# Kernel tuning notes

Hardware: AMD Instinct MI355X
Metric: run time of the kernel (lower is better)

Reference implementation:

```python
import jax, jax.numpy as jnp
import numpy as np

BETA = 0.05
KNN = 6
UL_ALPHA = 0.05
UL_BETA = 1.0


def setup_inputs() -> dict:
    key = jax.random.key(0)
    k1, k2, k3 = jax.random.split(key, 3)
    B, D, N = 256, 2048, 16384
    inputs = jax.random.normal(k1, (B, D), dtype=jnp.float32)
    em = jax.random.normal(k2, (N, D), dtype=jnp.float32)
    # exemplar memory rows are kept unit-norm by the update rule
    em = em / jnp.linalg.norm(em, axis=1, keepdims=True)
    targets = jax.random.randint(k3, (B,), 0, N, dtype=jnp.int64)
    return {"inputs": inputs, "em": em, "targets": targets, "epoch": 10}


def smooth_hot(logits, targets, em, k):
    # Vectorized k-reciprocal neighbor search (replaces the per-sample Python loop).
    m, n = logits.shape
    # index_sorted[:, :k] == top-k class indices per sample
    _, topk_idx = jax.lax.top_k(logits, k)            # [m, k]
    neigh = em[topk_idx]                               # [m, k, d]
    sims = jnp.einsum('mkd,nd->mkn', neigh, em)        # [m, k, n]
    _, neigh_topk = jax.lax.top_k(sims, k)             # [m, k, k]
    # neighbor j of sample i is reciprocal if anchor (top-1 of i) is in its top-k
    anchor = topk_idx[:, :1, None]                     # [m, 1, 1]
    recip = (neigh_topk == anchor).any(axis=-1)        # [m, k]
    weights = jnp.where(recip, 3.0 / k, 0.0).astype(logits.dtype)
    rows = jnp.arange(m)[:, None]
    onehot = jnp.zeros_like(logits).at[rows, topk_idx].set(weights)
    onehot = onehot.at[jnp.arange(m), targets].set(1.0)
    return onehot


def reference(inputs, em, targets, epoch):
    # ExemplarMemory.forward: similarity logits against the memory bank
    logits = (inputs @ em.T) / BETA                    # [B, N]
    # epoch >= 5 and knn > 0 branch (epoch=10)
    onehot = jax.lax.stop_gradient(
        smooth_hot(jax.lax.stop_gradient(logits), targets, em, KNN))
    logp = jax.nn.log_softmax(logits, axis=1)
    beta_loss = (-(onehot * logp).sum(axis=1)).mean()
    t_re = jnp.where(onehot == 0.0, jnp.float32(1e-4), onehot)
    alpha_loss = (-(jax.nn.softmax(logits, axis=1) * jnp.log(t_re)).sum(axis=1)).mean()
    return (UL_ALPHA * alpha_loss, UL_BETA * beta_loss)
```

## Files before the change

kernel.cpp:

```cpp
#include <hip/hip_runtime.h>
#include <math.h>

#define DIMK 2048
#define NEMB 16384
#define NB 256
#define NR2 1536
#define INV_BETA 20.0f
#define NEG_INF (-3.0e38f)

typedef short short8 __attribute__((ext_vector_type(8)));
typedef float f32x4 __attribute__((ext_vector_type(4)));

__device__ __forceinline__ unsigned short f2bf(float f) {
  unsigned u = __float_as_uint(f);
  u += 0x7fffu + ((u >> 16) & 1u);
  return (unsigned short)(u >> 16);
}

__device__ __forceinline__ void ins6i(float x, int xi, float v[6], int vi[6]) {
  if (x > v[5] || (x == v[5] && xi < vi[5])) {
    v[5] = x; vi[5] = xi;
#pragma unroll
    for (int j = 5; j > 0; j--) {
      if (v[j] > v[j - 1] || (v[j] == v[j - 1] && vi[j] < vi[j - 1])) {
        float tv = v[j]; v[j] = v[j - 1]; v[j - 1] = tv;
        int ti = vi[j]; vi[j] = vi[j - 1]; vi[j - 1] = ti;
      }
    }
  }
}

__global__ __launch_bounds__(256) void cvt_kernel(const float* __restrict__ src,
                                                  unsigned short* __restrict__ dst, int n4) {
  int i = blockIdx.x * 256 + threadIdx.x;
  if (i < n4) {
    float4 f = ((const float4*)src)[i];
    ushort4 o;
    o.x = f2bf(f.x); o.y = f2bf(f.y); o.z = f2bf(f.z); o.w = f2bf(f.w);
    ((ushort4*)dst)[i] = o;
  }
}

template <int MODE>
__global__ __launch_bounds__(256, 3) void gemm_rs(
    const unsigned short* __restrict__ Abase, const unsigned short* __restrict__ Bbase,
    const int* __restrict__ nidx, float* __restrict__ outC,
    const float* __restrict__ saIn, int* __restrict__ cntOut,
    const int* __restrict__ surv, const int* __restrict__ nsurvp) {
  constexpr int MTILE = (MODE == 0) ? 64 : 128;
  constexpr int MI = 4;
  constexpr int NI = (MODE == 0) ? 2 : 4;
  constexpr int NSUB_A = MTILE / 16;
  constexpr int NSUB = NSUB_A + 8;
  constexpr int NA = NSUB / 4;
  constexpr int NK = DIMK / 32;

  __shared__ unsigned short st[2][NSUB * 512];
  __shared__ int rowIdxSh[128];
  __shared__ float saSh[128];
  __shared__ int cntSh[128];
  __shared__ int outRowSh[128];
  int t = threadIdx.x;
  int lane = t & 63, wave = t >> 6;
  int quad = lane >> 4, l16 = lane & 15;
  int wr = (MODE == 0) ? 0 : (wave >> 1);
  int wc = (MODE == 0) ? wave : (wave & 1);
  int bn = blockIdx.x, bm = blockIdx.y;
  int nvalid = 128;

  if constexpr (MODE == 2) {
    int ns = nsurvp[0];
    if (bm * 128 >= ns) return;
    nvalid = (ns - bm * 128 < 128) ? (ns - bm * 128) : 128;
  }
  if constexpr (MODE >= 1) {
    if (t < 128) {
      int r;
      if constexpr (MODE == 1) r = bm * 128 + t;
      else r = surv[bm * 128 + ((t < nvalid) ? t : 0)];
      rowIdxSh[t] = nidx[r];
      saSh[t] = saIn[r];
      cntSh[t] = 0;
      outRowSh[t] = r;
    }
    __syncthreads();
  }

  int colbase = (MODE == 2) ? ((bn + 16) * 128) : (bn * 128);

  const unsigned short* agp[NA];
  int soff[NA];
  {
    int seg = lane >> 4;
#pragma unroll
    for (int a = 0; a < NA; a++) {
      int s = wave + a * 4;
      size_t grow;
      const unsigned short* basep;
      if (s < NSUB_A) {
        int r = s * 16 + l16;
        grow = (MODE == 0) ? (size_t)(bm * MTILE + r) : (size_t)rowIdxSh[r];
        basep = Abase;
      } else {
        grow = (size_t)(colbase + (s - NSUB_A) * 16 + l16);
        basep = Bbase;
      }
      agp[a] = basep + grow * DIMK + seg * 8;
      soff[a] = s * 512;
    }
  }

  f32x4 acc[MI][NI];
#pragma unroll
  for (int mi = 0; mi < MI; mi++)
#pragma unroll
    for (int ni = 0; ni < NI; ni++) acc[mi][ni] = (f32x4)0.0f;

  int lo = lane * 8;

  short8 rA[NA], rB2[NA];
  auto LOADT = [&](short8* R, int kk) {
#pragma unroll
    for (int a = 0; a < NA; a++) R[a] = *(const short8*)(agp[a] + kk * 32);
  };
  auto WRITET = [&](const short8* R, int b) {
#pragma unroll
    for (int a = 0; a < NA; a++) *(short8*)&st[b][soff[a] + lo] = R[a];
  };
  auto COMPUTE = [&](int b) {
    const unsigned short* hb = &st[b][0];
    short8 af[MI], bfv[NI];
#pragma unroll
    for (int mi = 0; mi < MI; mi++)
      af[mi] = *(const short8*)&hb[(wr * MI + mi) * 512 + lo];
#pragma unroll
    for (int ni = 0; ni < NI; ni++)
      bfv[ni] = *(const short8*)&hb[(NSUB_A + wc * NI + ni) * 512 + lo];
#pragma unroll
    for (int mi = 0; mi < MI; mi++)
#pragma unroll
      for (int ni = 0; ni < NI; ni++)
        acc[mi][ni] =
            __builtin_amdgcn_mfma_f32_16x16x32_bf16(af[mi], bfv[ni], acc[mi][ni], 0, 0, 0);
  };

  LOADT(rA, 0);
  LOADT(rB2, 1);
  WRITET(rA, 0);
  __syncthreads();

  for (int k = 0; k < NK; k += 2) {
    if (k + 2 < NK) LOADT(rA, k + 2);
    COMPUTE(0);
    WRITET(rB2, 1);
    __syncthreads();
    if (k + 3 < NK) LOADT(rB2, k + 3);
    COMPUTE(1);
    if (k + 2 < NK) WRITET(rA, 0);
    __syncthreads();
  }

  if constexpr (MODE == 0) {
#pragma unroll
    for (int mi = 0; mi < MI; mi++) {
      int row = bm * MTILE + mi * 16 + quad * 4;
#pragma unroll
      for (int ni = 0; ni < NI; ni++) {
        int col = bn * 128 + wave * 32 + ni * 16 + l16;
#pragma unroll
        for (int rr = 0; rr < 4; rr++)
          outC[(size_t)(row + rr) * NEMB + col] = acc[mi][ni][rr] * INV_BETA;
      }
    }
  } else {
#pragma unroll
    for (int mi = 0; mi < MI; mi++) {
#pragma unroll
      for (int rr = 0; rr < 4; rr++) {
        int rloc = wr * 64 + mi * 16 + quad * 4 + rr;
        float s = saSh[rloc];
        int c = 0;
#pragma unroll
        for (int ni = 0; ni < NI; ni++) c += (acc[mi][ni][rr] > s) ? 1 : 0;
        c += __shfl_xor(c, 1, 64);
        c += __shfl_xor(c, 2, 64);
        c += __shfl_xor(c, 4, 64);
        c += __shfl_xor(c, 8, 64);
        if (l16 == 0) atomicAdd(&cntSh[rloc], c);
      }
    }
    __syncthreads();
    if (t < nvalid) atomicAdd(&cntOut[outRowSh[t]], cntSh[t]);
  }
}

__global__ __launch_bounds__(256) void compact_kernel(const int* __restrict__ cnt,
                                                      int* __restrict__ surv,
                                                      int* __restrict__ nsurv) {
  __shared__ int ctr;
  if (threadIdx.x == 0) ctr = 0;
  __syncthreads();
  for (int i = threadIdx.x; i < NR2; i += 256) {
    if (cnt[i] < 6) {
      int p = atomicAdd(&ctr, 1);
      surv[p] = i;
    }
  }
  __syncthreads();
  if (threadIdx.x == 0) nsurv[0] = ctr;
}

__global__ __launch_bounds__(1024) void rowstats_kernel(
    const float* __restrict__ logits, float* __restrict__ topv,
    int* __restrict__ topi, float* __restrict__ lse) {
  int m = blockIdx.x, t = threadIdx.x;
  const float4* row4 = (const float4*)(logits + (size_t)m * NEMB);
  float v6[6]; int i6[6];
#pragma unroll
  for (int j = 0; j < 6; j++) { v6[j] = NEG_INF; i6[j] = 0x7fffffff; }
  float vals[16];
#pragma unroll
  for (int j = 0; j < 4; j++) {
    float4 f = row4[t + j * 1024];
    vals[j * 4 + 0] = f.x; vals[j * 4 + 1] = f.y;
    vals[j * 4 + 2] = f.z; vals[j * 4 + 3] = f.w;
  }
  float mx = vals[0];
#pragma unroll
  for (int r = 1; r < 16; r++) mx = fmaxf(mx, vals[r]);
  float sme = 0.f;
#pragma unroll
  for (int r = 0; r < 16; r++) sme += expf(vals[r] - mx);
#pragma unroll
  for (int j = 0; j < 4; j++) {
    int base = (t + j * 1024) * 4;
#pragma unroll
    for (int b = 0; b < 4; b++) ins6i(vals[j * 4 + b], base + b, v6, i6);
  }
  __shared__ float sv[1024 * 6]; __shared__ int si[1024 * 6];
  __shared__ float smx[1024], ssm[1024];
#pragma unroll
  for (int j = 0; j < 6; j++) { sv[t * 6 + j] = v6[j]; si[t * 6 + j] = i6[j]; }
  smx[t] = mx; ssm[t] = sme;
  __syncthreads();
  for (int s = 512; s > 0; s >>= 1) {
    if (t < s) {
      float mo = smx[t + s], lo2 = ssm[t + s];
      float mn = fmaxf(smx[t], mo);
      ssm[t] = ssm[t] * expf(smx[t] - mn) + lo2 * expf(mo - mn);
      smx[t] = mn;
#pragma unroll
      for (int j = 0; j < 6; j++) ins6i(sv[(t + s) * 6 + j], si[(t + s) * 6 + j], v6, i6);
#pragma unroll
      for (int j = 0; j < 6; j++) { sv[t * 6 + j] = v6[j]; si[t * 6 + j] = i6[j]; }
    }
    __syncthreads();
  }
  if (t == 0) {
    lse[m] = smx[0] + logf(ssm[0]);
#pragma unroll
    for (int j = 0; j < 6; j++) { topv[m * 6 + j] = v6[j]; topi[m * 6 + j] = i6[j]; }
  }
}

__global__ __launch_bounds__(256) void sa_kernel(const float* __restrict__ em,
                                                 const int* __restrict__ topi,
                                                 float* __restrict__ sa,
                                                 int* __restrict__ cnt) {
  int gid = blockIdx.x * 256 + threadIdx.x;
  int w = gid >> 6, lane = gid & 63;
  if (w >= NR2) return;
  if (lane == 1) cnt[w] = 0;
  int m = w / 6;
  int i = topi[w], a = topi[m * 6];
  const float* ei = em + (size_t)i * DIMK;
  const float* ea = em + (size_t)a * DIMK;
  float s = 0.f;
  for (int d = lane; d < DIMK; d += 64) s += ei[d] * ea[d];
#pragma unroll
  for (int off = 32; off > 0; off >>= 1) s += __shfl_down(s, off, 64);
  if (lane == 0) sa[w] = s;
}

__global__ __launch_bounds__(256) void final_kernel(
    const float* __restrict__ logits, const float* __restrict__ topv,
    const int* __restrict__ topi, const float* __restrict__ lse_arr,
    const int* __restrict__ cnt, const int* __restrict__ targets,
    float* __restrict__ out) {
  int m = threadIdx.x;
  float lse = lse_arr[m];
  int tgt = targets[m];
  float tl = logits[(size_t)m * NEMB + tgt];
  float beta = 0.f, Ps = 0.f, nbp = 0.f;
  bool tin = false;
#pragma unroll
  for (int k = 0; k < 6; k++) {
    int idx = topi[m * 6 + k]; float v = topv[m * 6 + k];
    float p = expf(v - lse);
    if (idx == tgt) { tin = true; beta += (lse - v); Ps += p; }
    else if (cnt[m * 6 + k] < 6) { beta += 0.5f * (lse - v); Ps += p; nbp += p; }
  }
  if (!tin) { beta += (lse - tl); Ps += expf(tl - lse); }
  float alpha = 9.2103404f * (1.f - Ps) + 0.6931472f * nbp;
  __shared__ float sA[256], sB2[256];
  sA[m] = alpha; sB2[m] = beta;
  __syncthreads();
  for (int s = 128; s > 0; s >>= 1) {
    if (m < s) { sA[m] += sA[m + s]; sB2[m] += sB2[m + s]; }
    __syncthreads();
  }
  if (m == 0) { out[0] = 0.05f * sA[0] / 256.f; out[1] = sB2[0] / 256.f; }
}

extern "C" void kernel_launch(void* const* d_in, const int* in_sizes, int n_in,
                              void* d_out, int out_size, void* d_ws, size_t ws_size,
                              hipStream_t stream) {
  const float* x = (const float*)d_in[0];
  const float* em = (const float*)d_in[1];
  const int* targets = (const int*)d_in[2];
  char* ws = (char*)d_ws;
  unsigned short* em_bf = (unsigned short*)ws;
  unsigned short* x_bf  = (unsigned short*)(ws + 67108864);
  float* logits = (float*)(ws + 68157440);
  int*   cnt    = (int*)  (ws + 84934656);
  int*   surv   = (int*)  (ws + 84940800);
  int*   nsurv  = (int*)  (ws + 84946944);
  float* topv   = (float*)(ws + 89653248);
  int*   topi   = (int*)  (ws + 89659392);
  float* lse    = (float*)(ws + 89665536);
  float* sa     = (float*)(ws + 89666560);

  cvt_kernel<<<dim3(32768), dim3(256), 0, stream>>>(em, em_bf, NEMB * DIMK / 4);
  cvt_kernel<<<dim3(512), dim3(256), 0, stream>>>(x, x_bf, NB * DIMK / 4);
  gemm_rs<0><<<dim3(128, 4), dim3(256), 0, stream>>>(
      x_bf, em_bf, (const int*)nullptr, logits, (const float*)nullptr, (int*)nullptr,
      (const int*)nullptr, (const int*)nullptr);
  rowstats_kernel<<<dim3(256), dim3(1024), 0, stream>>>(logits, topv, topi, lse);
  sa_kernel<<<dim3(384), dim3(256), 0, stream>>>(em, topi, sa, cnt);
  gemm_rs<1><<<dim3(16, 12), dim3(256), 0, stream>>>(
      em_bf, em_bf, topi, (float*)nullptr, sa, cnt, (const int*)nullptr,
      (const int*)nullptr);
  compact_kernel<<<dim3(1), dim3(256), 0, stream>>>(cnt, surv, nsurv);
  gemm_rs<2><<<dim3(112, 12), dim3(256), 0, stream>>>(
      em_bf, em_bf, topi, (float*)nullptr, sa, cnt, surv, nsurv);
  final_kernel<<<dim3(1), dim3(256), 0, stream>>>(logits, topv, topi, lse, cnt, targets,
                                                  (float*)d_out);
}
```

Baseline: 409.9 us.

## Split-K the three GEMMs with partial-sum planes and separate reduce/count kernels

Each GEMM now splits the K dimension across blockIdx.z (2, 4, and 2 slices) and writes fp32 partial results to separate planes instead of reducing in registers. New countA/countB kernels sum the partials and do the threshold counting, and rowstats sums the two logit planes and also captures the target logit. The goal is more blocks in flight for the small-grid GEMMs (192 blocks in mode 1) so the GPU is better filled. The cost is large extra global-memory traffic for the partial planes (hundreds of MB of workspace) plus extra kernel launches.

Result: slower. 468.1 us (+14.2%).

```diff
diff --git a/kernel.cpp b/kernel.cpp
--- a/kernel.cpp
+++ b/kernel.cpp
@@ -42,10 +42,9 @@
 }
 
 template <int MODE>
-__global__ __launch_bounds__(256, 3) void gemm_rs(
+__global__ __launch_bounds__(256, 3) void gemm_ks(
     const unsigned short* __restrict__ Abase, const unsigned short* __restrict__ Bbase,
-    const int* __restrict__ nidx, float* __restrict__ outC,
-    const float* __restrict__ saIn, int* __restrict__ cntOut,
+    const int* __restrict__ nidx, float* __restrict__ outP,
     const int* __restrict__ surv, const int* __restrict__ nsurvp) {
   constexpr int MTILE = (MODE == 0) ? 64 : 128;
   constexpr int MI = 4;
@@ -53,40 +52,36 @@
   constexpr int NSUB_A = MTILE / 16;
   constexpr int NSUB = NSUB_A + 8;
   constexpr int NA = NSUB / 4;
-  constexpr int NK = DIMK / 32;
+  constexpr int NKC = (MODE == 1) ? 16 : 32;
+  constexpr int OSTRIDE = (MODE == 0) ? 16384 : ((MODE == 1) ? 2048 : 14336);
+  constexpr size_t PLANE = (size_t)((MODE == 0) ? 256 : 1536) * OSTRIDE;
 
   __shared__ unsigned short st[2][NSUB * 512];
   __shared__ int rowIdxSh[128];
-  __shared__ float saSh[128];
-  __shared__ int cntSh[128];
-  __shared__ int outRowSh[128];
   int t = threadIdx.x;
   int lane = t & 63, wave = t >> 6;
   int quad = lane >> 4, l16 = lane & 15;
   int wr = (MODE == 0) ? 0 : (wave >> 1);
   int wc = (MODE == 0) ? wave : (wave & 1);
-  int bn = blockIdx.x, bm = blockIdx.y;
-  int nvalid = 128;
+  int bn = blockIdx.x, bm = blockIdx.y, kz = blockIdx.z;
 
   if constexpr (MODE == 2) {
     int ns = nsurvp[0];
     if (bm * 128 >= ns) return;
-    nvalid = (ns - bm * 128 < 128) ? (ns - bm * 128) : 128;
-  }
-  if constexpr (MODE >= 1) {
     if (t < 128) {
-      int r;
-      if constexpr (MODE == 1) r = bm * 128 + t;
-      else r = surv[bm * 128 + ((t < nvalid) ? t : 0)];
+      int idx = bm * 128 + t;
+      int r = surv[(idx < ns) ? idx : (bm * 128)];
       rowIdxSh[t] = nidx[r];
-      saSh[t] = saIn[r];
-      cntSh[t] = 0;
-      outRowSh[t] = r;
-    }
+    }
+    __syncthreads();
+  }
+  if constexpr (MODE == 1) {
+    if (t < 128) rowIdxSh[t] = nidx[bm * 128 + t];
     __syncthreads();
   }
 
   int colbase = (MODE == 2) ? ((bn + 16) * 128) : (bn * 128);
+  int kbase = kz * (NKC * 32);
 
   const unsigned short* agp[NA];
   int soff[NA];
@@ -105,7 +100,7 @@
         grow = (size_t)(colbase + (s - NSUB_A) * 16 + l16);
         basep = Bbase;
       }
-      agp[a] = basep + grow * DIMK + seg * 8;
+      agp[a] = basep + grow * DIMK + kbase + seg * 8;
       soff[a] = s * 512;
     }
   }
@@ -148,18 +143,18 @@
   LOADT(rB2, 1);
   WRITET(rA, 0);
   __syncthreads();
-
-  for (int k = 0; k < NK; k += 2) {
-    if (k + 2 < NK) LOADT(rA, k + 2);
+  for (int k = 0; k < NKC; k += 2) {
+    if (k + 2 < NKC) LOADT(rA, k + 2);
     COMPUTE(0);
     WRITET(rB2, 1);
     __syncthreads();
-    if (k + 3 < NK) LOADT(rB2, k + 3);
+    if (k + 3 < NKC) LOADT(rB2, k + 3);
     COMPUTE(1);
-    if (k + 2 < NK) WRITET(rA, 0);
-    __syncthreads();
-  }
-
+    if (k + 2 < NKC) WRITET(rA, 0);
+    __syncthreads();
+  }
+
+  float* op = outP + (size_t)kz * PLANE;
   if constexpr (MODE == 0) {
 #pragma unroll
     for (int mi = 0; mi < MI; mi++) {
@@ -169,28 +164,59 @@
         int col = bn * 128 + wave * 32 + ni * 16 + l16;
 #pragma unroll
         for (int rr = 0; rr < 4; rr++)
-          outC[(size_t)(row + rr) * NEMB + col] = acc[mi][ni][rr] * INV_BETA;
+          op[(size_t)(row + rr) * OSTRIDE + col] = acc[mi][ni][rr] * INV_BETA;
       }
     }
   } else {
 #pragma unroll
     for (int mi = 0; mi < MI; mi++) {
 #pragma unroll
-      for (int rr = 0; rr < 4; rr++) {
-        int rloc = wr * 64 + mi * 16 + quad * 4 + rr;
-        float s = saSh[rloc];
-        int c = 0;
-#pragma unroll
-        for (int ni = 0; ni < NI; ni++) c += (acc[mi][ni][rr] > s) ? 1 : 0;
-        c += __shfl_xor(c, 1, 64);
-        c += __shfl_xor(c, 2, 64);
-        c += __shfl_xor(c, 4, 64);
-        c += __shfl_xor(c, 8, 64);
-        if (l16 == 0) atomicAdd(&cntSh[rloc], c);
+      for (int ni = 0; ni < NI; ni++) {
+        int col = bn * 128 + wc * 64 + ni * 16 + l16;
+#pragma unroll
+        for (int rr = 0; rr < 4; rr++) {
+          int row = bm * 128 + wr * 64 + mi * 16 + quad * 4 + rr;
+          op[(size_t)row * OSTRIDE + col] = acc[mi][ni][rr];
+        }
       }
     }
-    __syncthreads();
-    if (t < nvalid) atomicAdd(&cntOut[outRowSh[t]], cntSh[t]);
+  }
+}
+
+__global__ __launch_bounds__(256) void countA_kernel(const float* __restrict__ simsA,
+                                                     const float* __restrict__ sa,
+                                                     int* __restrict__ cnt) {
+  int t = threadIdx.x, lane = t & 63;
+  constexpr size_t PL = (size_t)1536 * 2048;
+  for (int it = blockIdx.x; it < 1536 * 8; it += 256) {
+    int row = it >> 3, cx = it & 7;
+    size_t o = (size_t)row * 2048 + cx * 256 + t;
+    float s = simsA[o] + simsA[o + PL] + simsA[o + 2 * PL] + simsA[o + 3 * PL];
+    int c = (s > sa[row]) ? 1 : 0;
+#pragma unroll
+    for (int off = 32; off > 0; off >>= 1) c += __shfl_down(c, off, 64);
+    if (lane == 0 && c > 0) atomicAdd(&cnt[row], c);
+  }
+}
+
+__global__ __launch_bounds__(256) void countB_kernel(const float* __restrict__ simsB,
+                                                     const float* __restrict__ sa,
+                                                     const int* __restrict__ surv,
+                                                     const int* __restrict__ nsurvp,
+                                                     int* __restrict__ cnt) {
+  int t = threadIdx.x, lane = t & 63;
+  int ns = nsurvp[0];
+  constexpr size_t PL = (size_t)1536 * 14336;
+  int total = ns * 56;
+  for (int it = blockIdx.x; it < total; it += 448) {
+    int sv = it / 56, cx = it % 56;
+    size_t o = (size_t)sv * 14336 + cx * 256 + t;
+    float s = simsB[o] + simsB[o + PL];
+    int w = surv[sv];
+    int c = (s > sa[w]) ? 1 : 0;
+#pragma unroll
+    for (int off = 32; off > 0; off >>= 1) c += __shfl_down(c, off, 64);
+    if (lane == 0 && c > 0) atomicAdd(&cnt[w], c);
   }
 }
 
@@ -210,20 +236,24 @@
   if (threadIdx.x == 0) nsurv[0] = ctr;
 }
 
-__global__ __launch_bounds__(1024) void rowstats_kernel(
-    const float* __restrict__ logits, float* __restrict__ topv,
-    int* __restrict__ topi, float* __restrict__ lse) {
+__global__ __launch_bounds__(1024) void rowstats2_kernel(
+    const float* __restrict__ lpart, float* __restrict__ topv,
+    int* __restrict__ topi, float* __restrict__ lse,
+    const int* __restrict__ targets, float* __restrict__ tl) {
   int m = blockIdx.x, t = threadIdx.x;
-  const float4* row4 = (const float4*)(logits + (size_t)m * NEMB);
+  const float4* A4 = (const float4*)(lpart + (size_t)m * NEMB);
+  const float4* B4 = (const float4*)(lpart + (size_t)256 * NEMB + (size_t)m * NEMB);
+  int tgt = targets[m];
   float v6[6]; int i6[6];
 #pragma unroll
   for (int j = 0; j < 6; j++) { v6[j] = NEG_INF; i6[j] = 0x7fffffff; }
   float vals[16];
 #pragma unroll
   for (int j = 0; j < 4; j++) {
-    float4 f = row4[t + j * 1024];
-    vals[j * 4 + 0] = f.x; vals[j * 4 + 1] = f.y;
-    vals[j * 4 + 2] = f.z; vals[j * 4 + 3] = f.w;
+    float4 f = A4[t + j * 1024];
+    float4 g = B4[t + j * 1024];
+    vals[j * 4 + 0] = f.x + g.x; vals[j * 4 + 1] = f.y + g.y;
+    vals[j * 4 + 2] = f.z + g.z; vals[j * 4 + 3] = f.w + g.w;
   }
   float mx = vals[0];
 #pragma unroll
@@ -235,7 +265,11 @@
   for (int j = 0; j < 4; j++) {
     int base = (t + j * 1024) * 4;
 #pragma unroll
-    for (int b = 0; b < 4; b++) ins6i(vals[j * 4 + b], base + b, v6, i6);
+    for (int b = 0; b < 4; b++) {
+      int idx = base + b;
+      ins6i(vals[j * 4 + b], idx, v6, i6);
+      if (idx == tgt) tl[m] = vals[j * 4 + b];
+    }
   }
   __shared__ float sv[1024 * 6]; __shared__ int si[1024 * 6];
   __shared__ float smx[1024], ssm[1024];
@@ -283,14 +317,14 @@
 }
 
 __global__ __launch_bounds__(256) void final_kernel(
-    const float* __restrict__ logits, const float* __restrict__ topv,
+    const float* __restrict__ tl_arr, const float* __restrict__ topv,
     const int* __restrict__ topi, const float* __restrict__ lse_arr,
     const int* __restrict__ cnt, const int* __restrict__ targets,
     float* __restrict__ out) {
   int m = threadIdx.x;
   float lse = lse_arr[m];
   int tgt = targets[m];
-  float tl = logits[(size_t)m * NEMB + tgt];
+  float tlv = tl_arr[m];
   float beta = 0.f, Ps = 0.f, nbp = 0.f;
   bool tin = false;
 #pragma unroll
@@ -300,7 +334,7 @@
     if (idx == tgt) { tin = true; beta += (lse - v); Ps += p; }
     else if (cnt[m * 6 + k] < 6) { beta += 0.5f * (lse - v); Ps += p; nbp += p; }
   }
-  if (!tin) { beta += (lse - tl); Ps += expf(tl - lse); }
+  if (!tin) { beta += (lse - tlv); Ps += expf(tlv - lse); }
   float alpha = 9.2103404f * (1.f - Ps) + 0.6931472f * nbp;
   __shared__ float sA[256], sB2[256];
   sA[m] = alpha; sB2[m] = beta;
@@ -321,28 +355,31 @@
   char* ws = (char*)d_ws;
   unsigned short* em_bf = (unsigned short*)ws;
   unsigned short* x_bf  = (unsigned short*)(ws + 67108864);
-  float* logits = (float*)(ws + 68157440);
-  int*   cnt    = (int*)  (ws + 84934656);
-  int*   surv   = (int*)  (ws + 84940800);
-  int*   nsurv  = (int*)  (ws + 84946944);
-  float* topv   = (float*)(ws + 89653248);
-  int*   topi   = (int*)  (ws + 89659392);
-  float* lse    = (float*)(ws + 89665536);
-  float* sa     = (float*)(ws + 89666560);
+  float* lpart  = (float*)(ws + 68157440);
+  float* simsA  = (float*)(ws + 101711872);
+  float* simsB  = (float*)(ws + 152043520);
+  int*   cnt    = (int*)  (ws + 328204288);
+  int*   surv   = (int*)  (ws + 328210432);
+  int*   nsurv  = (int*)  (ws + 328216576);
+  float* topv   = (float*)(ws + 328216640);
+  int*   topi   = (int*)  (ws + 328222784);
+  float* lse    = (float*)(ws + 328228928);
+  float* sa     = (float*)(ws + 328229952);
+  float* tl     = (float*)(ws + 328236096);
 
   cvt_kernel<<<dim3(32768), dim3(256), 0, stream>>>(em, em_bf, NEMB * DIMK / 4);
   cvt_kernel<<<dim3(512), dim3(256), 0, stream>>>(x, x_bf, NB * DIMK / 4);
-  gemm_rs<0><<<dim3(128, 4), dim3(256), 0, stream>>>(
-      x_bf, em_bf, (const int*)nullptr, logits, (const float*)nullptr, (int*)nullptr,
-      (const int*)nullptr, (const int*)nullptr);
-  rowstats_kernel<<<dim3(256), dim3(1024), 0, stream>>>(logits, topv, topi, lse);
+  gemm_ks<0><<<dim3(128, 4, 2), dim3(256), 0, stream>>>(
+      x_bf, em_bf, (const int*)nullptr, lpart, (const int*)nullptr, (const int*)nullptr);
+  rowstats2_kernel<<<dim3(256), dim3(1024), 0, stream>>>(lpart, topv, topi, lse, targets, tl);
   sa_kernel<<<dim3(384), dim3(256), 0, stream>>>(em, topi, sa, cnt);
-  gemm_rs<1><<<dim3(16, 12), dim3(256), 0, stream>>>(
-      em_bf, em_bf, topi, (float*)nullptr, sa, cnt, (const int*)nullptr,
-      (const int*)nullptr);
+  gemm_ks<1><<<dim3(16, 12, 4), dim3(256), 0, stream>>>(
+      em_bf, em_bf, topi, simsA, (const int*)nullptr, (const int*)nullptr);
+  countA_kernel<<<dim3(256), dim3(256), 0, stream>>>(simsA, sa, cnt);
   compact_kernel<<<dim3(1), dim3(256), 0, stream>>>(cnt, surv, nsurv);
-  gemm_rs<2><<<dim3(112, 12), dim3(256), 0, stream>>>(
-      em_bf, em_bf, topi, (float*)nullptr, sa, cnt, surv, nsurv);
-  final_kernel<<<dim3(1), dim3(256), 0, stream>>>(logits, topv, topi, lse, cnt, targets,
+  gemm_ks<2><<<dim3(112, 12, 2), dim3(256), 0, stream>>>(
+      em_bf, em_bf, topi, simsB, surv, nsurv);
+  countB_kernel<<<dim3(448), dim3(256), 0, stream>>>(simsB, sa, surv, nsurv, cnt);
+  final_kernel<<<dim3(1), dim3(256), 0, stream>>>(tl, topv, topi, lse, cnt, targets,
                                                   (float*)d_out);
 }
```

## Split-K neighbor-similarity GEMMs with separate count kernels and skip anchor rows

Applied to the files above, without the earlier changes.

The neighbor-similarity GEMMs are split along K into four partial planes written to workspace, and new count kernels sum the planes and compare against the threshold. Anchor rows (every sixth slot) are dropped from the first pass and excluded from compaction. The second pass handles the first 256 survivors split-K, with an overflow MODE 3 path for the rest. The aim is more parallelism in the small-grid GEMMs, at the cost of extra global traffic for the partial planes and extra launches.

After: 414.7 us. About the same (+1.2%).

```diff
diff --git a/kernel.cpp b/kernel.cpp
--- a/kernel.cpp
+++ b/kernel.cpp
@@ -44,7 +44,7 @@
 template <int MODE>
 __global__ __launch_bounds__(256, 3) void gemm_rs(
     const unsigned short* __restrict__ Abase, const unsigned short* __restrict__ Bbase,
-    const int* __restrict__ nidx, float* __restrict__ outC,
+    const int* __restrict__ nidx, float* __restrict__ outP,
     const float* __restrict__ saIn, int* __restrict__ cntOut,
     const int* __restrict__ surv, const int* __restrict__ nsurvp) {
   constexpr int MTILE = (MODE == 0) ? 64 : 128;
@@ -53,7 +53,10 @@
   constexpr int NSUB_A = MTILE / 16;
   constexpr int NSUB = NSUB_A + 8;
   constexpr int NA = NSUB / 4;
-  constexpr int NK = DIMK / 32;
+  constexpr int NKC = (MODE == 1 || MODE == 2) ? 16 : 64;
+  constexpr int OSTRIDE = (MODE == 0) ? 16384 : ((MODE == 1) ? 2048 : 14336);
+  constexpr size_t PLANE =
+      (MODE == 1) ? (size_t)1280 * 2048 : ((MODE == 2) ? (size_t)256 * 14336 : 0);
 
   __shared__ unsigned short st[2][NSUB * 512];
   __shared__ int rowIdxSh[128];
@@ -65,19 +68,35 @@
   int quad = lane >> 4, l16 = lane & 15;
   int wr = (MODE == 0) ? 0 : (wave >> 1);
   int wc = (MODE == 0) ? wave : (wave & 1);
-  int bn = blockIdx.x, bm = blockIdx.y;
+  int bn = blockIdx.x, bm = blockIdx.y, kz = blockIdx.z;
   int nvalid = 128;
 
+  if constexpr (MODE == 1) {
+    if (t < 128) {
+      int slot = bm * 128 + t;
+      int g = (slot / 5) * 6 + (slot % 5) + 1;
+      rowIdxSh[t] = nidx[g];
+    }
+    __syncthreads();
+  }
   if constexpr (MODE == 2) {
     int ns = nsurvp[0];
-    if (bm * 128 >= ns) return;
-    nvalid = (ns - bm * 128 < 128) ? (ns - bm * 128) : 128;
-  }
-  if constexpr (MODE >= 1) {
+    int nsCap = (ns < 256) ? ns : 256;
+    if (bm * 128 >= nsCap) return;
     if (t < 128) {
-      int r;
-      if constexpr (MODE == 1) r = bm * 128 + t;
-      else r = surv[bm * 128 + ((t < nvalid) ? t : 0)];
+      int idx = bm * 128 + t;
+      rowIdxSh[t] = nidx[surv[(idx < nsCap) ? idx : 0]];
+    }
+    __syncthreads();
+  }
+  if constexpr (MODE == 3) {
+    int ns = nsurvp[0];
+    if (256 + bm * 128 >= ns) return;
+    nvalid = ns - 256 - bm * 128;
+    if (nvalid > 128) nvalid = 128;
+    if (t < 128) {
+      int idx = 256 + bm * 128 + ((t < nvalid) ? t : 0);
+      int r = surv[idx];
       rowIdxSh[t] = nidx[r];
       saSh[t] = saIn[r];
       cntSh[t] = 0;
@@ -86,7 +105,8 @@
     __syncthreads();
   }
 
-  int colbase = (MODE == 2) ? ((bn + 16) * 128) : (bn * 128);
+  int colbase = (MODE >= 2) ? ((bn + 16) * 128) : (bn * 128);
+  int kbase = (MODE == 1 || MODE == 2) ? kz * (NKC * 32) : 0;
 
   const unsigned short* agp[NA];
   int soff[NA];
@@ -105,7 +125,7 @@
         grow = (size_t)(colbase + (s - NSUB_A) * 16 + l16);
         basep = Bbase;
       }
-      agp[a] = basep + grow * DIMK + seg * 8;
+      agp[a] = basep + grow * DIMK + kbase + seg * 8;
       soff[a] = s * 512;
     }
   }
@@ -148,15 +168,14 @@
   LOADT(rB2, 1);
   WRITET(rA, 0);
   __syncthreads();
-
-  for (int k = 0; k < NK; k += 2) {
-    if (k + 2 < NK) LOADT(rA, k + 2);
+  for (int k = 0; k < NKC; k += 2) {
+    if (k + 2 < NKC) LOADT(rA, k + 2);
     COMPUTE(0);
     WRITET(rB2, 1);
     __syncthreads();
-    if (k + 3 < NK) LOADT(rB2, k + 3);
+    if (k + 3 < NKC) LOADT(rB2, k + 3);
     COMPUTE(1);
-    if (k + 2 < NK) WRITET(rA, 0);
+    if (k + 2 < NKC) WRITET(rA, 0);
     __syncthreads();
   }
 
@@ -169,7 +188,21 @@
         int col = bn * 128 + wave * 32 + ni * 16 + l16;
 #pragma unroll
         for (int rr = 0; rr < 4; rr++)
-          outC[(size_t)(row + rr) * NEMB + col] = acc[mi][ni][rr] * INV_BETA;
+          outP[(size_t)(row + rr) * OSTRIDE + col] = acc[mi][ni][rr] * INV_BETA;
+      }
+    }
+  } else if constexpr (MODE == 1 || MODE == 2) {
+    float* op = outP + (size_t)kz * PLANE;
+#pragma unroll
+    for (int mi = 0; mi < MI; mi++) {
+#pragma unroll
+      for (int ni = 0; ni < NI; ni++) {
+        int col = bn * 128 + wc * 64 + ni * 16 + l16;
+#pragma unroll
+        for (int rr = 0; rr < 4; rr++) {
+          int row = bm * 128 + wr * 64 + mi * 16 + quad * 4 + rr;
+          op[(size_t)row * OSTRIDE + col] = acc[mi][ni][rr];
+        }
       }
     }
   } else {
@@ -194,6 +227,45 @@
   }
 }
 
+__global__ __launch_bounds__(256) void countA_kernel(const float* __restrict__ simsA,
+                                                     const float* __restrict__ sa,
+                                                     int* __restrict__ cnt) {
+  int t = threadIdx.x, lane = t & 63;
+  constexpr size_t PL = (size_t)1280 * 2048;
+  for (int it = blockIdx.x; it < 1280 * 8; it += 256) {
+    int slot = it >> 3, cx = it & 7;
+    int g = (slot / 5) * 6 + (slot % 5) + 1;
+    size_t o = (size_t)slot * 2048 + cx * 256 + t;
+    float s = simsA[o] + simsA[o + PL] + simsA[o + 2 * PL] + simsA[o + 3 * PL];
+    int c = (s > sa[g]) ? 1 : 0;
+#pragma unroll
+    for (int off = 32; off > 0; off >>= 1) c += __shfl_down(c, off, 64);
+    if (lane == 0 && c > 0) atomicAdd(&cnt[g], c);
+  }
+}
+
+__global__ __launch_bounds__(256) void countB_kernel(const float* __restrict__ simsB,
+                                                     const float* __restrict__ sa,
+                                                     const int* __restrict__ surv,
+                                                     const int* __restrict__ nsurvp,
+                                                     int* __restrict__ cnt) {
+  int t = threadIdx.x, lane = t & 63;
+  int ns = nsurvp[0];
+  int nsCap = (ns < 256) ? ns : 256;
+  constexpr size_t PL = (size_t)256 * 14336;
+  int total = nsCap * 56;
+  for (int it = blockIdx.x; it < total; it += 448) {
+    int sv = it / 56, cx = it % 56;
+    size_t o = (size_t)sv * 14336 + cx * 256 + t;
+    float s = simsB[o] + simsB[o + PL] + simsB[o + 2 * PL] + simsB[o + 3 * PL];
+    int w = surv[sv];
+    int c = (s > sa[w]) ? 1 : 0;
+#pragma unroll
+    for (int off = 32; off > 0; off >>= 1) c += __shfl_down(c, off, 64);
+    if (lane == 0 && c > 0) atomicAdd(&cnt[w], c);
+  }
+}
+
 __global__ __launch_bounds__(256) void compact_kernel(const int* __restrict__ cnt,
                                                       int* __restrict__ surv,
                                                       int* __restrict__ nsurv) {
@@ -201,7 +273,7 @@
   if (threadIdx.x == 0) ctr = 0;
   __syncthreads();
   for (int i = threadIdx.x; i < NR2; i += 256) {
-    if (cnt[i] < 6) {
+    if ((i % 6) != 0 && cnt[i] < 6) {
       int p = atomicAdd(&ctr, 1);
       surv[p] = i;
     }
@@ -322,26 +394,32 @@
   unsigned short* em_bf = (unsigned short*)ws;
   unsigned short* x_bf  = (unsigned short*)(ws + 67108864);
   float* logits = (float*)(ws + 68157440);
-  int*   cnt    = (int*)  (ws + 84934656);
-  int*   surv   = (int*)  (ws + 84940800);
-  int*   nsurv  = (int*)  (ws + 84946944);
-  float* topv   = (float*)(ws + 89653248);
-  int*   topi   = (int*)  (ws + 89659392);
-  float* lse    = (float*)(ws + 89665536);
-  float* sa     = (float*)(ws + 89666560);
+  float* simsA  = (float*)(ws + 84934656);
+  float* simsB  = (float*)(ws + 126877696);
+  int*   cnt    = (int*)  (ws + 185597952);
+  int*   surv   = (int*)  (ws + 185604096);
+  int*   nsurv  = (int*)  (ws + 185610240);
+  float* topv   = (float*)(ws + 185610304);
+  int*   topi   = (int*)  (ws + 185616448);
+  float* lse    = (float*)(ws + 185622592);
+  float* sa     = (float*)(ws + 185623616);
 
   cvt_kernel<<<dim3(32768), dim3(256), 0, stream>>>(em, em_bf, NEMB * DIMK / 4);
   cvt_kernel<<<dim3(512), dim3(256), 0, stream>>>(x, x_bf, NB * DIMK / 4);
-  gemm_rs<0><<<dim3(128, 4), dim3(256), 0, stream>>>(
+  gemm_rs<0><<<dim3(128, 4, 1), dim3(256), 0, stream>>>(
       x_bf, em_bf, (const int*)nullptr, logits, (const float*)nullptr, (int*)nullptr,
       (const int*)nullptr, (const int*)nullptr);
   rowstats_kernel<<<dim3(256), dim3(1024), 0, stream>>>(logits, topv, topi, lse);
   sa_kernel<<<dim3(384), dim3(256), 0, stream>>>(em, topi, sa, cnt);
-  gemm_rs<1><<<dim3(16, 12), dim3(256), 0, stream>>>(
-      em_bf, em_bf, topi, (float*)nullptr, sa, cnt, (const int*)nullptr,
-      (const int*)nullptr);
+  gemm_rs<1><<<dim3(16, 10, 4), dim3(256), 0, stream>>>(
+      em_bf, em_bf, topi, simsA, (const float*)nullptr, (int*)nullptr,
+      (const int*)nullptr, (const int*)nullptr);
+  countA_kernel<<<dim3(256), dim3(256), 0, stream>>>(simsA, sa, cnt);
   compact_kernel<<<dim3(1), dim3(256), 0, stream>>>(cnt, surv, nsurv);
-  gemm_rs<2><<<dim3(112, 12), dim3(256), 0, stream>>>(
+  gemm_rs<2><<<dim3(112, 2, 4), dim3(256), 0, stream>>>(
+      em_bf, em_bf, topi, simsB, (const float*)nullptr, (int*)nullptr, surv, nsurv);
+  countB_kernel<<<dim3(448), dim3(256), 0, stream>>>(simsB, sa, surv, nsurv, cnt);
+  gemm_rs<3><<<dim3(112, 8, 1), dim3(256), 0, stream>>>(
       em_bf, em_bf, topi, (float*)nullptr, sa, cnt, surv, nsurv);
   final_kernel<<<dim3(1), dim3(256), 0, stream>>>(logits, topv, topi, lse, cnt, targets,
                                                   (float*)d_out);
```
